# Kernel tuning notes

Measured on AMD Instinct MI355X. Metric: run time of the kernel, lower is better.

The kernel has to match this reference:

```python
import jax, jax.numpy as jnp
import numpy as np

N = 100000  # nodes
E = 1000000  # edges
IN_DIM, HID_DIM, OUT_DIM = 64, 128, 2
BN_EPS = 1e-5


def sage_conv(x, src, dst, W_l, W_r, b, n_nodes):
    # PyG SAGEConv: out = lin_l(mean_{j in N(i)} x_j) + lin_r(x_i)
    msg = x[src]  # [E, d] gather
    agg = jax.ops.segment_sum(msg, dst, num_segments=n_nodes)  # [N, d]
    cnt = jax.ops.segment_sum(jnp.ones((src.shape[0],), x.dtype), dst, num_segments=n_nodes)
    agg = agg / jnp.maximum(cnt, 1.0)[:, None]  # mean aggregation
    return agg @ W_l + x @ W_r + b


def batch_norm(h, gamma, beta):
    # training-mode BatchNorm1d over the node dimension (biased variance)
    mu = h.mean(axis=0)
    var = h.var(axis=0)
    return (h - mu) * jax.lax.rsqrt(var + BN_EPS) * gamma + beta


def setup_inputs() -> dict:
    key = jax.random.key(0)
    ks = jax.random.split(key, 10)
    s = lambda fan_in: 1.0 / np.sqrt(fan_in)
    return {
        "x": jax.random.normal(ks[0], (N, IN_DIM), dtype=jnp.float32),
        "edge_index": jax.random.randint(ks[1], (2, E), 0, N, dtype=jnp.int64),
        "W1l": jax.random.uniform(ks[2], (IN_DIM, HID_DIM), jnp.float32, -s(IN_DIM), s(IN_DIM)),
        "W1r": jax.random.uniform(ks[3], (IN_DIM, HID_DIM), jnp.float32, -s(IN_DIM), s(IN_DIM)),
        "b1": jax.random.uniform(ks[4], (HID_DIM,), jnp.float32, -s(IN_DIM), s(IN_DIM)),
        "gamma": jnp.ones((HID_DIM,), jnp.float32),
        "beta": jnp.zeros((HID_DIM,), jnp.float32),
        "W2l": jax.random.uniform(ks[5], (HID_DIM, OUT_DIM), jnp.float32, -s(HID_DIM), s(HID_DIM)),
        "W2r": jax.random.uniform(ks[6], (HID_DIM, OUT_DIM), jnp.float32, -s(HID_DIM), s(HID_DIM)),
        "b2": jax.random.uniform(ks[7], (OUT_DIM,), jnp.float32, -s(HID_DIM), s(HID_DIM)),
    }


def reference(x, edge_index, W1l, W1r, b1, gamma, beta, W2l, W2r, b2):
    src, dst = edge_index[0], edge_index[1]
    h = sage_conv(x, src, dst, W1l, W1r, b1, x.shape[0])
    h = batch_norm(h, gamma, beta)
    h = jax.nn.relu(h)
    # dropout is identity in deterministic/eval reference
    return sage_conv(h, src, dst, W2l, W2r, b2, x.shape[0])
```

## Files before the change

kernel.cpp:

```cpp
#include <hip/hip_runtime.h>
#include <hip/hip_bf16.h>

#define NN 100000
#define NE 1000000
#define DIN 64
#define DH 128
#define NB 98
#define CAP 16384
#define NTILES 1563
#define EDGEB 256
#define CVTB 3125

typedef __attribute__((ext_vector_type(8))) short short8;
typedef __attribute__((ext_vector_type(4))) float floatx4;

#define OFF_BN    0
#define OFF_GCUR  256
#define OFF_OFFS  384
#define OFF_CSR   (OFF_OFFS + NN + 4)
#define OFF_PLR   (OFF_CSR + NE)
#define OFF_WF    (OFF_PLR + NN * 4)
#define OFF_AGB   (OFF_WF + 8192)
#define OFF_XB    (OFF_AGB + NN * 32)
#define OFF_H     (OFF_XB + NN * 32)

static __device__ __forceinline__ float b2f(short s) {
    union { unsigned u; float f; } c;
    c.u = ((unsigned)(unsigned short)s) << 16;
    return c.f;
}

__global__ __launch_bounds__(256) void k_bucketprep(const float* __restrict__ x,
                                                    const float* __restrict__ W1l,
                                                    const float* __restrict__ W1r,
                                                    const int* __restrict__ src,
                                                    const int* __restrict__ dst,
                                                    ushort* __restrict__ xb,
                                                    ushort* __restrict__ wfrag,
                                                    int* __restrict__ gcur,
                                                    int* __restrict__ ebuf) {
    const int bid = blockIdx.x;
    const int tid = threadIdx.x;
    if (bid < EDGEB) {
        __shared__ int lh[NB], lb[NB];
        const int per = (NE + EDGEB - 1) / EDGEB;
        const int e0 = bid * per, e1 = min(e0 + per, NE);
        if (tid < NB) lh[tid] = 0;
        __syncthreads();
        for (int e = e0 + tid; e < e1; e += 256)
            atomicAdd(&lh[dst[e] >> 10], 1);
        __syncthreads();
        if (tid < NB) { lb[tid] = atomicAdd(&gcur[tid], lh[tid]); lh[tid] = 0; }
        __syncthreads();
        for (int e = e0 + tid; e < e1; e += 256) {
            int d = dst[e];
            int b = d >> 10;
            int slot = b * CAP + lb[b] + atomicAdd(&lh[b], 1);
            ebuf[slot] = (src[e] << 10) | (d & 1023);
        }
    } else {
        int t = (bid - EDGEB) * 256 + tid;
        if (t < NN * DIN / 8) {
            float4 a = *(const float4*)(x + (size_t)t * 8);
            float4 b = *(const float4*)(x + (size_t)t * 8 + 4);
            __hip_bfloat16 o[8];
            o[0] = __float2bfloat16(a.x); o[1] = __float2bfloat16(a.y);
            o[2] = __float2bfloat16(a.z); o[3] = __float2bfloat16(a.w);
            o[4] = __float2bfloat16(b.x); o[5] = __float2bfloat16(b.y);
            o[6] = __float2bfloat16(b.z); o[7] = __float2bfloat16(b.w);
            *(uint4*)&xb[(size_t)t * 8] = *(uint4*)o;
        }
        if (t < 2048) {
            int ct = t >> 8, ks = (t >> 6) & 3, l = t & 63;
            int k0 = ks * 32 + (l >> 4) * 8;
            int col = ct * 16 + (l & 15);
            ushort o[8];
#pragma unroll
            for (int j = 0; j < 8; ++j) {
                int k = k0 + j;
                float v = (k < 64) ? W1l[k * DH + col] : W1r[(k - 64) * DH + col];
                __hip_bfloat16 b = __float2bfloat16(v);
                o[j] = *(ushort*)&b;
            }
            *(uint4*)&wfrag[(size_t)t * 8] = *(uint4*)o;
        }
    }
}

__global__ __launch_bounds__(1024) void k_place(const int* __restrict__ ebuf,
                                                const int* __restrict__ gcur,
                                                int* __restrict__ offs,
                                                int* __restrict__ csr) {
    __shared__ int lcnt[1024], loff[1024], pre[NB];
    __shared__ int sbase;
    const int b = blockIdx.x;
    const int tid = threadIdx.x;
    const int nb0 = b << 10;
    const int node_n = min(1024, NN - nb0);
    if (tid < NB) pre[tid] = gcur[tid];
    lcnt[tid] = 0;
    __syncthreads();
    if (tid == 0) {
        int acc = 0;
        for (int j = 0; j < b; ++j) acc += pre[j];
        sbase = acc;
    }
    const int e0 = b * CAP;
    const int ecnt = pre[b];
    for (int i = tid; i < ecnt; i += 1024)
        atomicAdd(&lcnt[ebuf[e0 + i] & 1023], 1);
    __syncthreads();
    int v = lcnt[tid];
    int sum = v;
    loff[tid] = sum;
    __syncthreads();
    for (int off = 1; off < 1024; off <<= 1) {
        int o = (tid >= off) ? loff[tid - off] : 0;
        __syncthreads();
        sum += o;
        loff[tid] = sum;
        __syncthreads();
    }
    const int excl = sum - v;
    const int base = sbase;
    if (tid < node_n) offs[nb0 + tid] = base + excl;
    if (b == NB - 1 && tid == 0) offs[NN] = NE;
    lcnt[tid] = 0;
    loff[tid] = excl;
    __syncthreads();
    for (int i = tid; i < ecnt; i += 1024) {
        int e = ebuf[e0 + i];
        int d = e & 1023;
        int slot = base + loff[d] + atomicAdd(&lcnt[d], 1);
        csr[slot] = e >> 10;
    }
}

__global__ __launch_bounds__(256) void k_aggv(const ushort* __restrict__ xb,
                                              const int* __restrict__ offs,
                                              const int* __restrict__ csr,
                                              ushort* __restrict__ aggb16) {
    int wid = (blockIdx.x * 256 + threadIdx.x) >> 6;
    int l = threadIdx.x & 63;
    if (wid >= NN) return;
    int beg = offs[wid];
    int deg = offs[wid + 1] - beg;
    const int g = l >> 3, d8 = l & 7;
    float a[8] = {0, 0, 0, 0, 0, 0, 0, 0};
    for (int ch = 0; ch < deg; ch += 8) {
        int j = ch + g;
        if (j < deg) {
            int sv = csr[beg + j];
            short8 v = *(const short8*)&xb[(size_t)sv * DIN + d8 * 8];
#pragma unroll
            for (int i = 0; i < 8; ++i) a[i] += b2f(v[i]);
        }
    }
#pragma unroll
    for (int i = 0; i < 8; ++i) {
        a[i] += __shfl_xor(a[i], 8);
        a[i] += __shfl_xor(a[i], 16);
        a[i] += __shfl_xor(a[i], 32);
    }
    if (g == 0) {
        float inv = 1.f / fmaxf((float)deg, 1.f);
        ushort o[8];
#pragma unroll
        for (int i = 0; i < 8; ++i) {
            __hip_bfloat16 b = __float2bfloat16(a[i] * inv);
            o[i] = *(ushort*)&b;
        }
        *(uint4*)&aggb16[(size_t)wid * DIN + d8 * 8] = *(uint4*)o;
    }
}

__global__ __launch_bounds__(256, 4) void k_mmx(const ushort* __restrict__ aggb16,
                                                const ushort* __restrict__ xb,
                                                const ushort* __restrict__ wfrag,
                                                const float* __restrict__ b1,
                                                ushort* __restrict__ hb,
                                                float* __restrict__ bnsum,
                                                float* __restrict__ bnsq) {
    __shared__ ushort sA[64 * 136];
    const int tid = threadIdx.x;
    const int l = tid & 63, w = tid >> 6;
    const int r0 = l & 15, kg = l >> 4;

    short8 bf[2][4];
#pragma unroll
    for (int c = 0; c < 2; ++c)
#pragma unroll
        for (int ks = 0; ks < 4; ++ks)
            bf[c][ks] = *(const short8*)&wfrag[(((2 * w + c) * 4 + ks) * 64 + l) * 8];

    float bias2[2];
    bias2[0] = b1[(2 * w) * 16 + r0];
    bias2[1] = b1[(2 * w + 1) * 16 + r0];

    float psum2[2] = {0.f, 0.f}, psq2[2] = {0.f, 0.f};

    for (int tile = blockIdx.x; tile < NTILES; tile += gridDim.x) {
        const int tb = tile * 64;
        __syncthreads();
#pragma unroll
        for (int i = 0; i < 4; ++i) {
            int f = tid + i * 256;
            int row = f >> 4, ch = f & 15;
            const uint4* src = (ch < 8)
                ? (const uint4*)(aggb16 + (size_t)(tb + row) * 64 + ch * 8)
                : (const uint4*)(xb + (size_t)(tb + row) * 64 + (ch - 8) * 8);
            *(uint4*)&sA[row * 136 + ch * 8] = *src;
        }
        __syncthreads();

#pragma unroll
        for (int s = 0; s < 4; ++s) {
            short8 af[4];
            const int abase = (s * 16 + r0) * 136 + kg * 8;
#pragma unroll
            for (int ks = 0; ks < 4; ++ks)
                af[ks] = *(const short8*)&sA[abase + ks * 32];
#pragma unroll
            for (int c = 0; c < 2; ++c) {
                floatx4 acc = {0.f, 0.f, 0.f, 0.f};
#pragma unroll
                for (int ks = 0; ks < 4; ++ks)
                    acc = __builtin_amdgcn_mfma_f32_16x16x32_bf16(af[ks], bf[c][ks], acc, 0, 0, 0);
                const int col = (2 * w + c) * 16 + r0;
#pragma unroll
                for (int i = 0; i < 4; ++i) {
                    int r = tb + s * 16 + kg * 4 + i;
                    if (r < NN) {
                        float o = acc[i] + bias2[c];
                        __hip_bfloat16 ob = __float2bfloat16(o);
                        hb[(size_t)r * DH + col] = *(ushort*)&ob;
                        psum2[c] += o;
                        psq2[c] += o * o;
                    }
                }
            }
        }
    }

#pragma unroll
    for (int c = 0; c < 2; ++c) {
        float s = psum2[c], q = psq2[c];
        s += __shfl_xor(s, 16); s += __shfl_xor(s, 32);
        q += __shfl_xor(q, 16); q += __shfl_xor(q, 32);
        if (kg == 0) {
            atomicAdd(&bnsum[(2 * w + c) * 16 + r0], s);
            atomicAdd(&bnsq[(2 * w + c) * 16 + r0], q);
        }
    }
}

__global__ __launch_bounds__(256) void k_proj(const ushort* __restrict__ hb,
                                              const float* __restrict__ bnsum,
                                              const float* __restrict__ bnsq,
                                              const float* __restrict__ gamma,
                                              const float* __restrict__ beta,
                                              const float* __restrict__ W2l,
                                              const float* __restrict__ W2r,
                                              float4* __restrict__ plr) {
    __shared__ float sCA[DH], sCC[DH];
    int tid = threadIdx.x;
    if (tid < DH) {
        float mu = bnsum[tid] * (1.f / NN);
        float var = bnsq[tid] * (1.f / NN) - mu * mu;
        float a = rsqrtf(var + 1e-5f) * gamma[tid];
        sCA[tid] = a;
        sCC[tid] = beta[tid] - mu * a;
    }
    __syncthreads();
    int wid = (blockIdx.x * 256 + tid) >> 6;
    int lane = tid & 63;
    if (wid >= NN) return;
    int c0 = lane * 2;
    uint hv = *(const uint*)&hb[(size_t)wid * DH + c0];
    float h0 = b2f((short)(hv & 0xffff));
    float h1 = b2f((short)(hv >> 16));
    float hb0 = fmaxf(h0 * sCA[c0] + sCC[c0], 0.f);
    float hb1 = fmaxf(h1 * sCA[c0 + 1] + sCC[c0 + 1], 0.f);
    float pl0 = hb0 * W2l[c0 * 2 + 0] + hb1 * W2l[c0 * 2 + 2];
    float pl1 = hb0 * W2l[c0 * 2 + 1] + hb1 * W2l[c0 * 2 + 3];
    float pr0 = hb0 * W2r[c0 * 2 + 0] + hb1 * W2r[c0 * 2 + 2];
    float pr1 = hb0 * W2r[c0 * 2 + 1] + hb1 * W2r[c0 * 2 + 3];
#pragma unroll
    for (int off = 32; off > 0; off >>= 1) {
        pl0 += __shfl_down(pl0, off);
        pl1 += __shfl_down(pl1, off);
        pr0 += __shfl_down(pr0, off);
        pr1 += __shfl_down(pr1, off);
    }
    if (lane == 0) plr[wid] = make_float4(pl0, pl1, pr0, pr1);
}

__global__ __launch_bounds__(256) void k_out(const float4* __restrict__ plr,
                                             const int* __restrict__ offs,
                                             const int* __restrict__ csr,
                                             const float* __restrict__ b2,
                                             float* __restrict__ out) {
    int d = blockIdx.x * 256 + threadIdx.x;
    if (d >= NN) return;
    int beg = offs[d];
    int deg = offs[d + 1] - beg;
    const float2* pl2 = (const float2*)plr;
    float s0 = 0.f, s1 = 0.f;
    int i = 0;
    for (; i + 4 <= deg; i += 4) {
        int n0 = csr[beg + i], n1 = csr[beg + i + 1];
        int n2 = csr[beg + i + 2], n3 = csr[beg + i + 3];
        float2 p0 = pl2[(size_t)n0 * 2];
        float2 p1 = pl2[(size_t)n1 * 2];
        float2 p2 = pl2[(size_t)n2 * 2];
        float2 p3 = pl2[(size_t)n3 * 2];
        s0 += (p0.x + p1.x) + (p2.x + p3.x);
        s1 += (p0.y + p1.y) + (p2.y + p3.y);
    }
    for (; i < deg; ++i) {
        float2 p = pl2[(size_t)csr[beg + i] * 2];
        s0 += p.x;
        s1 += p.y;
    }
    float inv = 1.f / fmaxf((float)deg, 1.f);
    float4 me = plr[d];
    out[(size_t)d * 2 + 0] = s0 * inv + me.z + b2[0];
    out[(size_t)d * 2 + 1] = s1 * inv + me.w + b2[1];
}

extern "C" void kernel_launch(void* const* d_in, const int* in_sizes, int n_in,
                              void* d_out, int out_size, void* d_ws, size_t ws_size,
                              hipStream_t stream) {
    const float* x = (const float*)d_in[0];
    const int* ei = (const int*)d_in[1];
    const float* W1l = (const float*)d_in[2];
    const float* W1r = (const float*)d_in[3];
    const float* b1 = (const float*)d_in[4];
    const float* gamma = (const float*)d_in[5];
    const float* beta = (const float*)d_in[6];
    const float* W2l = (const float*)d_in[7];
    const float* W2r = (const float*)d_in[8];
    const float* b2 = (const float*)d_in[9];
    float* out = (float*)d_out;
    float* ws = (float*)d_ws;
    int* wsi = (int*)d_ws;

    const int* src = ei;
    const int* dst = ei + NE;

    float* bnsum = ws + OFF_BN;
    float* bnsq = ws + OFF_BN + 128;
    int* gcur = wsi + OFF_GCUR;
    int* offs = wsi + OFF_OFFS;
    int* csr = wsi + OFF_CSR;
    float4* plr = (float4*)(ws + OFF_PLR);
    ushort* wfrag = (ushort*)(ws + OFF_WF);
    ushort* aggb16 = (ushort*)(ws + OFF_AGB);
    ushort* xb = (ushort*)(ws + OFF_XB);
    ushort* hb = (ushort*)(ws + OFF_H);
    int* ebuf = (int*)(ws + OFF_H);

    hipMemsetAsync(ws, 0, (256 + NB) * sizeof(float), stream);

    k_bucketprep<<<EDGEB + CVTB, 256, 0, stream>>>(x, W1l, W1r, src, dst, xb, wfrag, gcur, ebuf);
    k_place<<<NB, 1024, 0, stream>>>(ebuf, gcur, offs, csr);
    k_aggv<<<(NN * 64 + 255) / 256, 256, 0, stream>>>(xb, offs, csr, aggb16);
    k_mmx<<<782, 256, 0, stream>>>(aggb16, xb, wfrag, b1, hb, bnsum, bnsq);
    k_proj<<<(NN + 3) / 4, 256, 0, stream>>>(hb, bnsum, bnsq, gamma, beta, W2l, W2r, plr);
    k_out<<<(NN + 255) / 256, 256, 0, stream>>>(plr, offs, csr, b2, out);
}
```

Baseline: 224.9 us.

## Fuse neighbor mean aggregation into layer-1 MFMA GEMM kernel

Merges the separate gather-mean kernel and the MFMA GEMM kernel into one. Each 64-node tile block now aggregates its own neighbors straight into shared memory next to the self features, then runs the matrix multiply. This removes the global round-trip through the bf16 aggregate buffer and one kernel launch. In exchange, each wave handles 16 nodes one after another, which may lower memory-level parallelism in the gather, and the grid changes from a persistent 782-block loop to one block per tile.

```diff
diff --git a/kernel.cpp b/kernel.cpp
--- a/kernel.cpp
+++ b/kernel.cpp
@@ -20,8 +20,7 @@
 #define OFF_CSR   (OFF_OFFS + NN + 4)
 #define OFF_PLR   (OFF_CSR + NE)
 #define OFF_WF    (OFF_PLR + NN * 4)
-#define OFF_AGB   (OFF_WF + 8192)
-#define OFF_XB    (OFF_AGB + NN * 32)
+#define OFF_XB    (OFF_WF + 8192)
 #define OFF_H     (OFF_XB + NN * 32)
 
 static __device__ __forceinline__ float b2f(short s) {
@@ -136,55 +135,20 @@
     }
 }
 
-__global__ __launch_bounds__(256) void k_aggv(const ushort* __restrict__ xb,
-                                              const int* __restrict__ offs,
-                                              const int* __restrict__ csr,
-                                              ushort* __restrict__ aggb16) {
-    int wid = (blockIdx.x * 256 + threadIdx.x) >> 6;
-    int l = threadIdx.x & 63;
-    if (wid >= NN) return;
-    int beg = offs[wid];
-    int deg = offs[wid + 1] - beg;
-    const int g = l >> 3, d8 = l & 7;
-    float a[8] = {0, 0, 0, 0, 0, 0, 0, 0};
-    for (int ch = 0; ch < deg; ch += 8) {
-        int j = ch + g;
-        if (j < deg) {
-            int sv = csr[beg + j];
-            short8 v = *(const short8*)&xb[(size_t)sv * DIN + d8 * 8];
-#pragma unroll
-            for (int i = 0; i < 8; ++i) a[i] += b2f(v[i]);
-        }
-    }
-#pragma unroll
-    for (int i = 0; i < 8; ++i) {
-        a[i] += __shfl_xor(a[i], 8);
-        a[i] += __shfl_xor(a[i], 16);
-        a[i] += __shfl_xor(a[i], 32);
-    }
-    if (g == 0) {
-        float inv = 1.f / fmaxf((float)deg, 1.f);
-        ushort o[8];
-#pragma unroll
-        for (int i = 0; i < 8; ++i) {
-            __hip_bfloat16 b = __float2bfloat16(a[i] * inv);
-            o[i] = *(ushort*)&b;
-        }
-        *(uint4*)&aggb16[(size_t)wid * DIN + d8 * 8] = *(uint4*)o;
-    }
-}
-
-__global__ __launch_bounds__(256, 4) void k_mmx(const ushort* __restrict__ aggb16,
-                                                const ushort* __restrict__ xb,
-                                                const ushort* __restrict__ wfrag,
-                                                const float* __restrict__ b1,
-                                                ushort* __restrict__ hb,
-                                                float* __restrict__ bnsum,
-                                                float* __restrict__ bnsq) {
+__global__ __launch_bounds__(256, 4) void k_aggmm(const ushort* __restrict__ xb,
+                                                  const int* __restrict__ offs,
+                                                  const int* __restrict__ csr,
+                                                  const ushort* __restrict__ wfrag,
+                                                  const float* __restrict__ b1,
+                                                  ushort* __restrict__ hb,
+                                                  float* __restrict__ bnsum,
+                                                  float* __restrict__ bnsq) {
     __shared__ ushort sA[64 * 136];
     const int tid = threadIdx.x;
     const int l = tid & 63, w = tid >> 6;
     const int r0 = l & 15, kg = l >> 4;
+    const int g = l >> 3, d8 = l & 7;
+    const int tb = blockIdx.x * 64;
 
     short8 bf[2][4];
 #pragma unroll
@@ -197,46 +161,75 @@
     bias2[0] = b1[(2 * w) * 16 + r0];
     bias2[1] = b1[(2 * w + 1) * 16 + r0];
 
+#pragma unroll
+    for (int i = 0; i < 2; ++i) {
+        int f = tid + i * 256;
+        int row = f >> 3, c8 = f & 7;
+        *(uint4*)&sA[row * 136 + 64 + c8 * 8] =
+            *(const uint4*)&xb[(size_t)(tb + row) * DIN + c8 * 8];
+    }
+
+#pragma unroll 2
+    for (int nn = 0; nn < 16; ++nn) {
+        int node = tb + w * 16 + nn;
+        float a[8] = {0, 0, 0, 0, 0, 0, 0, 0};
+        int deg = 0;
+        if (node < NN) {
+            int beg = offs[node];
+            deg = offs[node + 1] - beg;
+            for (int ch = 0; ch < deg; ch += 8) {
+                int j = ch + g;
+                if (j < deg) {
+                    int sv = csr[beg + j];
+                    short8 v = *(const short8*)&xb[(size_t)sv * DIN + d8 * 8];
+#pragma unroll
+                    for (int i = 0; i < 8; ++i) a[i] += b2f(v[i]);
+                }
+            }
+        }
+#pragma unroll
+        for (int i = 0; i < 8; ++i) {
+            a[i] += __shfl_xor(a[i], 8);
+            a[i] += __shfl_xor(a[i], 16);
+            a[i] += __shfl_xor(a[i], 32);
+        }
+        if (g == 0) {
+            float inv = 1.f / fmaxf((float)deg, 1.f);
+            ushort o[8];
+#pragma unroll
+            for (int i = 0; i < 8; ++i) {
+                __hip_bfloat16 b = __float2bfloat16(a[i] * inv);
+                o[i] = *(ushort*)&b;
+            }
+            *(uint4*)&sA[(w * 16 + nn) * 136 + d8 * 8] = *(uint4*)o;
+        }
+    }
+    __syncthreads();
+
     float psum2[2] = {0.f, 0.f}, psq2[2] = {0.f, 0.f};
-
-    for (int tile = blockIdx.x; tile < NTILES; tile += gridDim.x) {
-        const int tb = tile * 64;
-        __syncthreads();
-#pragma unroll
-        for (int i = 0; i < 4; ++i) {
-            int f = tid + i * 256;
-            int row = f >> 4, ch = f & 15;
-            const uint4* src = (ch < 8)
-                ? (const uint4*)(aggb16 + (size_t)(tb + row) * 64 + ch * 8)
-                : (const uint4*)(xb + (size_t)(tb + row) * 64 + (ch - 8) * 8);
-            *(uint4*)&sA[row * 136 + ch * 8] = *src;
-        }
-        __syncthreads();
-
-#pragma unroll
-        for (int s = 0; s < 4; ++s) {
-            short8 af[4];
-            const int abase = (s * 16 + r0) * 136 + kg * 8;
+#pragma unroll
+    for (int s = 0; s < 4; ++s) {
+        short8 af[4];
+        const int abase = (s * 16 + r0) * 136 + kg * 8;
+#pragma unroll
+        for (int ks = 0; ks < 4; ++ks)
+            af[ks] = *(const short8*)&sA[abase + ks * 32];
+#pragma unroll
+        for (int c = 0; c < 2; ++c) {
+            floatx4 acc = {0.f, 0.f, 0.f, 0.f};
 #pragma unroll
             for (int ks = 0; ks < 4; ++ks)
-                af[ks] = *(const short8*)&sA[abase + ks * 32];
-#pragma unroll
-            for (int c = 0; c < 2; ++c) {
-                floatx4 acc = {0.f, 0.f, 0.f, 0.f};
-#pragma unroll
-                for (int ks = 0; ks < 4; ++ks)
-                    acc = __builtin_amdgcn_mfma_f32_16x16x32_bf16(af[ks], bf[c][ks], acc, 0, 0, 0);
-                const int col = (2 * w + c) * 16 + r0;
-#pragma unroll
-                for (int i = 0; i < 4; ++i) {
-                    int r = tb + s * 16 + kg * 4 + i;
-                    if (r < NN) {
-                        float o = acc[i] + bias2[c];
-                        __hip_bfloat16 ob = __float2bfloat16(o);
-                        hb[(size_t)r * DH + col] = *(ushort*)&ob;
-                        psum2[c] += o;
-                        psq2[c] += o * o;
-                    }
+                acc = __builtin_amdgcn_mfma_f32_16x16x32_bf16(af[ks], bf[c][ks], acc, 0, 0, 0);
+            const int col = (2 * w + c) * 16 + r0;
+#pragma unroll
+            for (int i = 0; i < 4; ++i) {
+                int r = tb + s * 16 + kg * 4 + i;
+                if (r < NN) {
+                    float o = acc[i] + bias2[c];
+                    __hip_bfloat16 ob = __float2bfloat16(o);
+                    hb[(size_t)r * DH + col] = *(ushort*)&ob;
+                    psum2[c] += o;
+                    psq2[c] += o * o;
                 }
             }
         }
@@ -355,7 +348,6 @@
     int* csr = wsi + OFF_CSR;
     float4* plr = (float4*)(ws + OFF_PLR);
     ushort* wfrag = (ushort*)(ws + OFF_WF);
-    ushort* aggb16 = (ushort*)(ws + OFF_AGB);
     ushort* xb = (ushort*)(ws + OFF_XB);
     ushort* hb = (ushort*)(ws + OFF_H);
     int* ebuf = (int*)(ws + OFF_H);
@@ -364,8 +356,7 @@
 
     k_bucketprep<<<EDGEB + CVTB, 256, 0, stream>>>(x, W1l, W1r, src, dst, xb, wfrag, gcur, ebuf);
     k_place<<<NB, 1024, 0, stream>>>(ebuf, gcur, offs, csr);
-    k_aggv<<<(NN * 64 + 255) / 256, 256, 0, stream>>>(xb, offs, csr, aggb16);
-    k_mmx<<<782, 256, 0, stream>>>(aggb16, xb, wfrag, b1, hb, bnsum, bnsq);
+    k_aggmm<<<NTILES, 256, 0, stream>>>(xb, offs, csr, wfrag, b1, hb, bnsum, bnsq);
     k_proj<<<(NN + 3) / 4, 256, 0, stream>>>(hb, bnsum, bnsq, gamma, beta, W2l, W2r, plr);
     k_out<<<(NN + 255) / 256, 256, 0, stream>>>(plr, offs, csr, b2, out);
 }
```

After: 251.6 us. 1.12x slower.
